# Kernel tuning notes

Measured on AMD Instinct MI355X. Metric: run time of the kernel, lower is better.

## Reference

```python
import jax, jax.numpy as jnp
import numpy as np

E = 1_000_000   # total edges across batch
B = 1024        # n_batch (graphs)
IN = 128
OUT = 128


def setup_inputs() -> dict:
    key = jax.random.key(0)
    ks = jax.random.split(key, 8)
    x1 = jax.random.normal(ks[0], (E, IN), dtype=jnp.float32)
    # cumulative slice boundaries: [0, sorted interior cuts, E]
    inner = jnp.sort(jax.random.randint(ks[1], (B - 1,), 0, E))
    edge_slices = jnp.concatenate([jnp.zeros((1,), jnp.int32),
                                   inner.astype(jnp.int32),
                                   jnp.full((1,), E, jnp.int32)])
    s1 = 1.0 / np.sqrt(IN)
    s2 = 1.0 / np.sqrt(OUT)
    W1 = jax.random.uniform(ks[2], (IN, OUT), jnp.float32, -s1, s1)
    b1 = jax.random.uniform(ks[3], (OUT,), jnp.float32, -s1, s1)
    W2 = jax.random.uniform(ks[4], (OUT, OUT), jnp.float32, -s2, s2)
    b2 = jax.random.uniform(ks[5], (OUT,), jnp.float32, -s2, s2)
    W3 = jax.random.uniform(ks[6], (OUT, OUT), jnp.float32, -s2, s2)
    b3 = jax.random.uniform(ks[7], (OUT,), jnp.float32, -s2, s2)
    return {"x1": x1, "edge_slices": edge_slices,
            "W1": W1, "b1": b1, "W2": W2, "b2": b2, "W3": W3, "b3": b3}


def reference(x1, edge_slices, W1, b1, W2, b2, W3, b3):
    n_edges = x1.shape[0]
    n_batch = edge_slices.shape[0] - 1
    # internal MLP: Linear -> ReLU -> Linear
    h = jax.nn.relu(x1 @ W1 + b1) @ W2 + b2  # [E, OUT]
    # segment id of edge i: index of slice containing i (replaces repeat_interleave)
    seg = jnp.searchsorted(edge_slices[1:], jnp.arange(n_edges), side='right')
    sums = jax.ops.segment_sum(h, seg, num_segments=n_batch)        # [B, OUT]
    counts = (edge_slices[1:] - edge_slices[:-1]).astype(h.dtype)   # [B]
    mean = sums / jnp.maximum(counts, 1.0)[:, None]  # empty segments -> 0 (matches scatter-mean)
    # external MLP: single Linear
    return mean @ W3 + b3
```

## Files before the change

kernel.cpp:

```cpp
#include <hip/hip_runtime.h>
#include <hip/hip_bf16.h>

typedef __attribute__((ext_vector_type(8))) short short8;
typedef __attribute__((ext_vector_type(4))) float floatx4;
typedef unsigned short u16;
typedef unsigned int u32;

#define TM 128
#define D 128
#define LDSX 136
#define LDSG 132

static __device__ __forceinline__ u16 f2bf(float f) {
  union { float f; u32 u; } v; v.f = f;
  u32 r = v.u + 0x7fffu + ((v.u >> 16) & 1u);
  return (u16)(r >> 16);
}

__global__ void prep_kernel(const float* __restrict__ W1, u16* __restrict__ W1T,
                            float* __restrict__ S, int nS)
{
  int t = blockIdx.x * blockDim.x + threadIdx.x;
  if (t < D * D) {
    int k = t >> 7;
    int n = t & (D - 1);
    W1T[n * D + k] = f2bf(W1[t]);
  }
  if (t < nS) S[t] = 0.f;
}

__global__ __launch_bounds__(256, 2)
void fused_mlp_segsum(const float* __restrict__ x1,
                      const int* __restrict__ slices,
                      const u16* __restrict__ W1T,
                      const float* __restrict__ b1,
                      float* __restrict__ S,
                      int E, int B)
{
  __shared__ __align__(16) char smem[2 * TM * LDSX * 2];
  __shared__ float partial[4 * D];
  u16* xt = (u16*)smem;
  u16* wt = (u16*)smem + TM * LDSX;
  float* g = (float*)smem;

  const int tid = threadIdx.x;
  const int r0 = blockIdx.x * TM;

  #pragma unroll
  for (int i = 0; i < 8; ++i) {
    int f = tid + i * 256;
    int n = f >> 4;
    int c = (f & 15) * 8;
    uint4 w = *(const uint4*)(W1T + n * D + c);
    *(uint4*)(wt + n * LDSX + c) = w;
  }
  #pragma unroll
  for (int i = 0; i < 16; ++i) {
    int f = tid + i * 256;
    int r = f >> 5;
    int c = (f & 31) * 4;
    int row = r0 + r;
    float4 v;
    if (row < E) v = *(const float4*)(x1 + (size_t)row * D + c);
    else         v = make_float4(0.f, 0.f, 0.f, 0.f);
    uint2 pk;
    pk.x = (u32)f2bf(v.x) | ((u32)f2bf(v.y) << 16);
    pk.y = (u32)f2bf(v.z) | ((u32)f2bf(v.w) << 16);
    *(uint2*)(xt + r * LDSX + c) = pk;
  }
  __syncthreads();

  const int wave = tid >> 6;
  const int lane = tid & 63;
  const int quad = lane >> 4;
  const int l16  = lane & 15;

  floatx4 acc[2][8];
  #pragma unroll
  for (int a = 0; a < 2; ++a)
    #pragma unroll
    for (int b = 0; b < 8; ++b)
      acc[a][b] = (floatx4){0.f, 0.f, 0.f, 0.f};

  #pragma unroll
  for (int kk = 0; kk < 4; ++kk) {
    int ko = kk * 32 + quad * 8;
    short8 a0 = *(const short8*)(xt + (wave * 32 +      l16) * LDSX + ko);
    short8 a1 = *(const short8*)(xt + (wave * 32 + 16 + l16) * LDSX + ko);
    #pragma unroll
    for (int ct = 0; ct < 8; ++ct) {
      short8 b = *(const short8*)(wt + (ct * 16 + l16) * LDSX + ko);
      acc[0][ct] = __builtin_amdgcn_mfma_f32_16x16x32_bf16(a0, b, acc[0][ct], 0, 0, 0);
      acc[1][ct] = __builtin_amdgcn_mfma_f32_16x16x32_bf16(a1, b, acc[1][ct], 0, 0, 0);
    }
  }

  __syncthreads();

  #pragma unroll
  for (int ct = 0; ct < 8; ++ct) {
    float bias = b1[ct * 16 + l16];
    #pragma unroll
    for (int rt = 0; rt < 2; ++rt) {
      #pragma unroll
      for (int i = 0; i < 4; ++i) {
        float v = acc[rt][ct][i] + bias;
        v = fmaxf(v, 0.f);
        int row = wave * 32 + rt * 16 + quad * 4 + i;
        g[row * LDSG + ct * 16 + l16] = v;
      }
    }
  }
  __syncthreads();

  int l = 0, r = B + 1;
  while (l < r) { int m = (l + r) >> 1; if (slices[m] <= r0) l = m + 1; else r = m; }
  int s0 = l - 1;

  const int rEnd = min(r0 + TM, E);
  const int c2 = (tid & 63) * 2;
  const int rg = tid >> 6;

  for (int s = s0; s < B && slices[s] < rEnd; ++s) {
    int lo = max(slices[s], r0) - r0;
    int hi = min(slices[s + 1], rEnd) - r0;
    if (hi <= lo) continue;
    float ax = 0.f, ay = 0.f;
    for (int rr = lo + rg; rr < hi; rr += 4) {
      float2 v = *(const float2*)(g + rr * LDSG + c2);
      ax += v.x; ay += v.y;
    }
    partial[rg * D + c2]     = ax;
    partial[rg * D + c2 + 1] = ay;
    __syncthreads();
    if (tid < D) {
      float t = partial[tid] + partial[D + tid] + partial[2 * D + tid] + partial[3 * D + tid];
      atomicAdd(&S[(size_t)s * D + tid], t);
    }
    __syncthreads();
  }
}

__global__ __launch_bounds__(128)
void finish_mlp(const float* __restrict__ S, const int* __restrict__ slices,
                const float* __restrict__ W2, const float* __restrict__ b2,
                const float* __restrict__ W3, const float* __restrict__ b3,
                float* __restrict__ out, int B)
{
  __shared__ float v0[D];
  __shared__ float v1[D];
  int s = blockIdx.x;
  int j = threadIdx.x;
  int c0 = slices[s], c1 = slices[s + 1];
  int cnt = c1 - c0;
  if (cnt <= 0) { out[s * D + j] = b3[j]; return; }
  v0[j] = S[s * D + j] * (1.f / (float)cnt);
  __syncthreads();
  float a = b2[j];
  #pragma unroll 8
  for (int k = 0; k < D; ++k) a = fmaf(v0[k], W2[k * D + j], a);
  v1[j] = a;
  __syncthreads();
  float o = b3[j];
  #pragma unroll 8
  for (int k = 0; k < D; ++k) o = fmaf(v1[k], W3[k * D + j], o);
  out[s * D + j] = o;
}

extern "C" void kernel_launch(void* const* d_in, const int* in_sizes, int n_in,
                              void* d_out, int out_size, void* d_ws, size_t ws_size,
                              hipStream_t stream) {
  const float* x1     = (const float*)d_in[0];
  const int*   slices = (const int*)d_in[1];
  const float* W1     = (const float*)d_in[2];
  const float* b1     = (const float*)d_in[3];
  const float* W2     = (const float*)d_in[4];
  const float* b2     = (const float*)d_in[5];
  const float* W3     = (const float*)d_in[6];
  const float* b3     = (const float*)d_in[7];
  float* out = (float*)d_out;

  const int E = in_sizes[0] / D;
  const int B = in_sizes[1] - 1;

  float* S   = (float*)d_ws;
  u16*   W1T = (u16*)((char*)d_ws + (size_t)B * D * 4);

  int nS = B * D;
  prep_kernel<<<(nS + 255) / 256, 256, 0, stream>>>(W1, W1T, S, nS);

  int nblk = (E + TM - 1) / TM;
  fused_mlp_segsum<<<nblk, 256, 0, stream>>>(x1, slices, W1T, b1, S, E, B);

  finish_mlp<<<B, D, 0, stream>>>(S, slices, W2, b2, W3, b3, out, B);
}
```

Measured before the change: 776.0 us.

## Persistent multi-tile blocks with register-held W1, double-buffered x prefetch, in-register segment sums

Each block now processes a chunk of four 64-row tiles instead of one 128-row tile. W1 fragments are kept in registers per wave rather than reloaded into LDS, and the next tile's x rows are prefetched into registers and converted into a double-buffered LDS slot while the current tile computes. Segment sums accumulate directly from MFMA accumulators in registers, reduced with shuffles, and flushed with atomics only when a segment ends. This removes the LDS round-trip for the hidden activations and the per-segment barriers, and it raises the occupancy target. The cost is more register pressure and serialized segment-walk logic per tile.

```diff
diff --git a/kernel.cpp b/kernel.cpp
--- a/kernel.cpp
+++ b/kernel.cpp
@@ -6,10 +6,11 @@
 typedef unsigned short u16;
 typedef unsigned int u32;
 
-#define TM 128
 #define D 128
+#define TM 64
+#define NT 4
+#define CHUNK (TM*NT)
 #define LDSX 136
-#define LDSG 132
 
 static __device__ __forceinline__ u16 f2bf(float f) {
   union { float f; u32 u; } v; v.f = f;
@@ -29,7 +30,7 @@
   if (t < nS) S[t] = 0.f;
 }
 
-__global__ __launch_bounds__(256, 2)
+__global__ __launch_bounds__(256, 3)
 void fused_mlp_segsum(const float* __restrict__ x1,
                       const int* __restrict__ slices,
                       const u16* __restrict__ W1T,
@@ -37,107 +38,160 @@
                       float* __restrict__ S,
                       int E, int B)
 {
-  __shared__ __align__(16) char smem[2 * TM * LDSX * 2];
-  __shared__ float partial[4 * D];
-  u16* xt = (u16*)smem;
-  u16* wt = (u16*)smem + TM * LDSX;
-  float* g = (float*)smem;
-
-  const int tid = threadIdx.x;
-  const int r0 = blockIdx.x * TM;
-
-  #pragma unroll
-  for (int i = 0; i < 8; ++i) {
-    int f = tid + i * 256;
-    int n = f >> 4;
-    int c = (f & 15) * 8;
-    uint4 w = *(const uint4*)(W1T + n * D + c);
-    *(uint4*)(wt + n * LDSX + c) = w;
-  }
-  #pragma unroll
-  for (int i = 0; i < 16; ++i) {
-    int f = tid + i * 256;
-    int r = f >> 5;
-    int c = (f & 31) * 4;
-    int row = r0 + r;
-    float4 v;
-    if (row < E) v = *(const float4*)(x1 + (size_t)row * D + c);
-    else         v = make_float4(0.f, 0.f, 0.f, 0.f);
-    uint2 pk;
-    pk.x = (u32)f2bf(v.x) | ((u32)f2bf(v.y) << 16);
-    pk.y = (u32)f2bf(v.z) | ((u32)f2bf(v.w) << 16);
-    *(uint2*)(xt + r * LDSX + c) = pk;
-  }
-  __syncthreads();
-
-  const int wave = tid >> 6;
+  __shared__ __align__(16) u16 xt[2][TM * LDSX];
+
+  const int tid  = threadIdx.x;
+  const int wv   = tid >> 6;
   const int lane = tid & 63;
   const int quad = lane >> 4;
   const int l16  = lane & 15;
 
-  floatx4 acc[2][8];
+  const int chunkStart = blockIdx.x * CHUNK;
+  const int chunkEnd   = min(chunkStart + CHUNK, E);
+  const int ntiles     = (chunkEnd - chunkStart + TM - 1) / TM;
+
+  short8 bf[2][4];
   #pragma unroll
-  for (int a = 0; a < 2; ++a)
-    #pragma unroll
-    for (int b = 0; b < 8; ++b)
-      acc[a][b] = (floatx4){0.f, 0.f, 0.f, 0.f};
-
-  #pragma unroll
-  for (int kk = 0; kk < 4; ++kk) {
-    int ko = kk * 32 + quad * 8;
-    short8 a0 = *(const short8*)(xt + (wave * 32 +      l16) * LDSX + ko);
-    short8 a1 = *(const short8*)(xt + (wave * 32 + 16 + l16) * LDSX + ko);
-    #pragma unroll
-    for (int ct = 0; ct < 8; ++ct) {
-      short8 b = *(const short8*)(wt + (ct * 16 + l16) * LDSX + ko);
-      acc[0][ct] = __builtin_amdgcn_mfma_f32_16x16x32_bf16(a0, b, acc[0][ct], 0, 0, 0);
-      acc[1][ct] = __builtin_amdgcn_mfma_f32_16x16x32_bf16(a1, b, acc[1][ct], 0, 0, 0);
-    }
-  }
-
+  for (int c = 0; c < 2; ++c)
+    #pragma unroll
+    for (int kk = 0; kk < 4; ++kk)
+      bf[c][kk] = *(const short8*)(W1T + ((2 * wv + c) * 16 + l16) * D + kk * 32 + quad * 8);
+
+  float bias[2] = { b1[wv * 32 + l16], b1[wv * 32 + 16 + l16] };
+
+  int l = 0, r = B + 1;
+  while (l < r) { int m = (l + r) >> 1; if (slices[m] <= chunkStart) l = m + 1; else r = m; }
+  int cur = l - 1;
+  float racc0 = 0.f, racc1 = 0.f;
+
+  {
+    #pragma unroll
+    for (int i = 0; i < 8; ++i) {
+      int f = tid + i * 256;
+      int row = chunkStart + (f >> 5);
+      int c = (f & 31) * 4;
+      int rr = min(row, E - 1);
+      float4 v = *(const float4*)(x1 + (size_t)rr * D + c);
+      if (row >= E) { v.x = 0.f; v.y = 0.f; v.z = 0.f; v.w = 0.f; }
+      uint2 pk;
+      pk.x = (u32)f2bf(v.x) | ((u32)f2bf(v.y) << 16);
+      pk.y = (u32)f2bf(v.z) | ((u32)f2bf(v.w) << 16);
+      *(uint2*)(&xt[0][(f >> 5) * LDSX + c]) = pk;
+    }
+  }
   __syncthreads();
 
-  #pragma unroll
-  for (int ct = 0; ct < 8; ++ct) {
-    float bias = b1[ct * 16 + l16];
-    #pragma unroll
-    for (int rt = 0; rt < 2; ++rt) {
-      #pragma unroll
-      for (int i = 0; i < 4; ++i) {
-        float v = acc[rt][ct][i] + bias;
-        v = fmaxf(v, 0.f);
-        int row = wave * 32 + rt * 16 + quad * 4 + i;
-        g[row * LDSG + ct * 16 + l16] = v;
-      }
-    }
-  }
-  __syncthreads();
-
-  int l = 0, r = B + 1;
-  while (l < r) { int m = (l + r) >> 1; if (slices[m] <= r0) l = m + 1; else r = m; }
-  int s0 = l - 1;
-
-  const int rEnd = min(r0 + TM, E);
-  const int c2 = (tid & 63) * 2;
-  const int rg = tid >> 6;
-
-  for (int s = s0; s < B && slices[s] < rEnd; ++s) {
-    int lo = max(slices[s], r0) - r0;
-    int hi = min(slices[s + 1], rEnd) - r0;
-    if (hi <= lo) continue;
-    float ax = 0.f, ay = 0.f;
-    for (int rr = lo + rg; rr < hi; rr += 4) {
-      float2 v = *(const float2*)(g + rr * LDSG + c2);
-      ax += v.x; ay += v.y;
-    }
-    partial[rg * D + c2]     = ax;
-    partial[rg * D + c2 + 1] = ay;
+  for (int t = 0; t < ntiles; ++t) {
+    const int base = chunkStart + t * TM;
+
+    float4 ld[8];
+    const bool havePf = (t + 1 < ntiles);
+    if (havePf) {
+      int nb = base + TM;
+      #pragma unroll
+      for (int i = 0; i < 8; ++i) {
+        int f = tid + i * 256;
+        int row = nb + (f >> 5);
+        int rr = min(row, E - 1);
+        ld[i] = *(const float4*)(x1 + (size_t)rr * D + (f & 31) * 4);
+        if (row >= E) { ld[i].x = 0.f; ld[i].y = 0.f; ld[i].z = 0.f; ld[i].w = 0.f; }
+      }
+    }
+
+    const u16* xb = xt[t & 1];
+    floatx4 acc[4][2];
+    #pragma unroll
+    for (int rt = 0; rt < 4; ++rt)
+      #pragma unroll
+      for (int c = 0; c < 2; ++c)
+        acc[rt][c] = (floatx4){0.f, 0.f, 0.f, 0.f};
+
+    #pragma unroll
+    for (int kk = 0; kk < 4; ++kk) {
+      #pragma unroll
+      for (int rt = 0; rt < 4; ++rt) {
+        short8 a = *(const short8*)(xb + (rt * 16 + l16) * LDSX + kk * 32 + quad * 8);
+        acc[rt][0] = __builtin_amdgcn_mfma_f32_16x16x32_bf16(a, bf[0][kk], acc[rt][0], 0, 0, 0);
+        acc[rt][1] = __builtin_amdgcn_mfma_f32_16x16x32_bf16(a, bf[1][kk], acc[rt][1], 0, 0, 0);
+      }
+    }
+
+    #pragma unroll
+    for (int rt = 0; rt < 4; ++rt)
+      #pragma unroll
+      for (int c = 0; c < 2; ++c)
+        #pragma unroll
+        for (int i = 0; i < 4; ++i)
+          acc[rt][c][i] = fmaxf(acc[rt][c][i] + bias[c], 0.f);
+
+    const int tileHi = min(base + TM, chunkEnd);
+
+    auto segAdd = [&](int loR, int hiR) {
+      #pragma unroll
+      for (int rt = 0; rt < 4; ++rt)
+        #pragma unroll
+        for (int i = 0; i < 4; ++i) {
+          int rowOff = rt * 16 + quad * 4 + i;
+          bool in = (rowOff >= loR) && (rowOff < hiR);
+          racc0 += in ? acc[rt][0][i] : 0.f;
+          racc1 += in ? acc[rt][1][i] : 0.f;
+        }
+    };
+    auto flushSeg = [&](int s) {
+      float t0 = racc0, t1 = racc1;
+      t0 += __shfl_xor(t0, 16); t0 += __shfl_xor(t0, 32);
+      t1 += __shfl_xor(t1, 16); t1 += __shfl_xor(t1, 32);
+      if (quad == 0) {
+        atomicAdd(&S[s * D + wv * 32 + l16], t0);
+        atomicAdd(&S[s * D + wv * 32 + 16 + l16], t1);
+      }
+    };
+
+    while (cur < B) {
+      int segEnd = slices[cur + 1];
+      if (segEnd > tileHi) break;
+      int lo = max(slices[cur], base);
+      if (segEnd > lo) segAdd(lo - base, segEnd - base);
+      flushSeg(cur);
+      racc0 = 0.f; racc1 = 0.f;
+      ++cur;
+    }
+    if (cur < B) {
+      int lo = max(slices[cur], base);
+      if (lo < tileHi) {
+        if (lo == base && tileHi == base + TM) {
+          #pragma unroll
+          for (int rt = 0; rt < 4; ++rt)
+            #pragma unroll
+            for (int i = 0; i < 4; ++i) { racc0 += acc[rt][0][i]; racc1 += acc[rt][1][i]; }
+        } else {
+          segAdd(lo - base, tileHi - base);
+        }
+      }
+    }
+
+    if (havePf) {
+      u16* dst = xt[(t + 1) & 1];
+      #pragma unroll
+      for (int i = 0; i < 8; ++i) {
+        int f = tid + i * 256;
+        uint2 pk;
+        pk.x = (u32)f2bf(ld[i].x) | ((u32)f2bf(ld[i].y) << 16);
+        pk.y = (u32)f2bf(ld[i].z) | ((u32)f2bf(ld[i].w) << 16);
+        *(uint2*)(&dst[(f >> 5) * LDSX + (f & 31) * 4]) = pk;
+      }
+    }
     __syncthreads();
-    if (tid < D) {
-      float t = partial[tid] + partial[D + tid] + partial[2 * D + tid] + partial[3 * D + tid];
-      atomicAdd(&S[(size_t)s * D + tid], t);
-    }
-    __syncthreads();
+  }
+
+  if (cur < B && slices[cur] < chunkEnd) {
+    float t0 = racc0, t1 = racc1;
+    t0 += __shfl_xor(t0, 16); t0 += __shfl_xor(t0, 32);
+    t1 += __shfl_xor(t1, 16); t1 += __shfl_xor(t1, 32);
+    if (quad == 0) {
+      atomicAdd(&S[cur * D + wv * 32 + l16], t0);
+      atomicAdd(&S[cur * D + wv * 32 + 16 + l16], t1);
+    }
   }
 }
 
@@ -189,7 +243,7 @@
   int nS = B * D;
   prep_kernel<<<(nS + 255) / 256, 256, 0, stream>>>(W1, W1T, S, nS);
 
-  int nblk = (E + TM - 1) / TM;
+  int nblk = (E + CHUNK - 1) / CHUNK;
   fused_mlp_segsum<<<nblk, 256, 0, stream>>>(x1, slices, W1T, b1, S, E, B);
 
   finish_mlp<<<B, D, 0, stream>>>(S, slices, W2, b2, W3, b3, out, B);
```

Measured after the change: 675.2 us. 1.15x faster.
